# Kernel tuning notes

Measured on AMD Instinct MI355X. Metric: run time of the kernel, lower is better.

## Reference

```python
import jax, jax.numpy as jnp
import numpy as np

B, N, C = 2, 4096, 1024   # batch, input_size (seq), channels
H, Dh = 16, 64            # nhead, head_dim = channels // nhead
K = 256                   # dim_k (Linformer projected length)
FF = 4096                 # dim_ff
DEPTH = 2
EPS = 1e-5


def setup_inputs() -> dict:
    key = jax.random.key(0)
    ks = jax.random.split(key, 16)
    s = 0.02
    return {
        "x": jax.random.normal(ks[0], (B, N, C), jnp.float32),
        # per-layer, per-head Q/K/V projections: Linear(channels -> head_dim, bias=False)
        "Wq": jax.random.normal(ks[1], (DEPTH, H, C, Dh), jnp.float32) * s,
        "Wk": jax.random.normal(ks[2], (DEPTH, H, C, Dh), jnp.float32) * s,
        "Wv": jax.random.normal(ks[3], (DEPTH, H, C, Dh), jnp.float32) * s,
        # output proj: Linear(nhead*head_dim -> channels) with bias
        "Wo": jax.random.normal(ks[4], (DEPTH, H * Dh, C), jnp.float32) * s,
        "bo": jax.random.normal(ks[5], (DEPTH, C), jnp.float32) * s,
        # layerwise-shared E_proj = Linear(input_size -> dim_k) applied along seq axis
        # (same object used for both K and V projections)
        "Ew": jax.random.normal(ks[6], (K, N), jnp.float32) * (1.0 / np.sqrt(N)),
        "Eb": jax.random.normal(ks[7], (K,), jnp.float32) * s,
        # FeedForward: Linear(C->FF), gelu, Linear(FF->C)
        "W1": jax.random.normal(ks[8], (DEPTH, C, FF), jnp.float32) * s,
        "b1": jax.random.normal(ks[9], (DEPTH, FF), jnp.float32) * s,
        "W2": jax.random.normal(ks[10], (DEPTH, FF, C), jnp.float32) * s,
        "b2": jax.random.normal(ks[11], (DEPTH, C), jnp.float32) * s,
        # post-residual LayerNorm params: [layer, {attn, ff}, channels]
        "ln_g": 1.0 + 0.02 * jax.random.normal(ks[12], (DEPTH, 2, C), jnp.float32),
        "ln_b": 0.02 * jax.random.normal(ks[13], (DEPTH, 2, C), jnp.float32),
    }


def _layernorm(x, g, b):
    mu = jnp.mean(x, axis=-1, keepdims=True)
    var = jnp.var(x, axis=-1, keepdims=True)
    return (x - mu) * jax.lax.rsqrt(var + EPS) * g + b


def reference(x, Wq, Wk, Wv, Wo, bo, Ew, Eb, W1, b1, W2, b2, ln_g, ln_b):
    scale = 1.0 / np.sqrt(Dh)
    for l in range(DEPTH):
        # ---- Linformer multi-head attention (dropout = identity at inference) ----
        q = jnp.einsum('bnc,hcd->bhnd', x, Wq[l])   # [B,H,N,Dh]
        k = jnp.einsum('bnc,hcd->bhnd', x, Wk[l])
        v = jnp.einsum('bnc,hcd->bhnd', x, Wv[l])
        # project seq axis n -> k with shared E_proj (K^T @ E, V^T @ E)
        kp = jnp.einsum('bhnd,kn->bhkd', k, Ew) + Eb[None, None, :, None]  # [B,H,K,Dh]
        vp = jnp.einsum('bhnd,kn->bhkd', v, Ew) + Eb[None, None, :, None]
        p = jax.nn.softmax(jnp.einsum('bhnd,bhkd->bhnk', q, kp) * scale, axis=-1)
        o = jnp.einsum('bhnk,bhkd->bhnd', p, vp)
        o = o.transpose(0, 2, 1, 3).reshape(B, N, H * Dh)  # concat heads
        attn_out = o @ Wo[l] + bo[l]
        x = _layernorm(x + attn_out, ln_g[l, 0], ln_b[l, 0])  # Residual post-norm
        # ---- FeedForward ----
        h = jax.nn.gelu(x @ W1[l] + b1[l], approximate=False)
        ff_out = h @ W2[l] + b2[l]
        x = _layernorm(x + ff_out, ln_g[l, 1], ln_b[l, 1])
    return x
```

## Files before the change

### kernel.cpp

```cpp
#include <hip/hip_runtime.h>
#include <hip/hip_bf16.h>
#include <math.h>

typedef __bf16 bf16x8 __attribute__((ext_vector_type(8)));
typedef float f32x4 __attribute__((ext_vector_type(4)));

__global__ void cvt_f32_bf16(const float* __restrict__ in, __bf16* __restrict__ out, long n) {
    long i = ((long)blockIdx.x * 256 + threadIdx.x) * 4;
    long stride = (long)gridDim.x * 1024;
    for (; i < n; i += stride) {
        float4 v = *(const float4*)(in + i);
        out[i + 0] = (__bf16)v.x;
        out[i + 1] = (__bf16)v.y;
        out[i + 2] = (__bf16)v.z;
        out[i + 3] = (__bf16)v.w;
    }
}

__global__ void transpose_cvt(const float* __restrict__ in, __bf16* __restrict__ out,
                              int ldin, int ldout, long inBS, long outBS) {
    __shared__ __bf16 tile[32][33];
    in  += (long)blockIdx.z * inBS;
    out += (long)blockIdx.z * outBS;
    int n0 = blockIdx.x * 32, m0 = blockIdx.y * 32;
    for (int i = threadIdx.y; i < 32; i += 8)
        tile[i][threadIdx.x] = (__bf16)in[(long)(m0 + i) * ldin + n0 + threadIdx.x];
    __syncthreads();
    for (int i = threadIdx.y; i < 32; i += 8)
        out[(long)(n0 + i) * ldout + m0 + threadIdx.x] = tile[threadIdx.x][i];
}

__global__ void transpose_bf16(const __bf16* __restrict__ in, __bf16* __restrict__ out,
                               int rows, int cols) {
    __shared__ __bf16 tile[32][33];
    in  += (long)blockIdx.z * rows * cols;
    out += (long)blockIdx.z * rows * cols;
    int c0 = blockIdx.x * 32, r0 = blockIdx.y * 32;
    for (int i = threadIdx.y; i < 32; i += 8)
        tile[i][threadIdx.x] = in[(long)(r0 + i) * cols + c0 + threadIdx.x];
    __syncthreads();
    for (int i = threadIdx.y; i < 32; i += 8)
        out[(long)(c0 + i) * rows + r0 + threadIdx.x] = tile[threadIdx.x][i];
}

template<bool COLB, bool GELUF, bool RES, int OUT>
__global__ __launch_bounds__(512, 2) void gemm8p(
    const __bf16* __restrict__ A, int lda,
    const __bf16* __restrict__ Bt, int ldb,
    void* __restrict__ outp, int ldc,
    const float* __restrict__ colBias,
    const float* __restrict__ res, int ldres,
    int K)
{
    __shared__ __bf16 Asm[2][16384];
    __shared__ __bf16 Bsm[2][16384];

    const int tid = threadIdx.x, lane = tid & 63, wave = tid >> 6;
    const int l15 = lane & 15, l4 = lane >> 4;
    const int wm = wave >> 2, wn = wave & 3;

    int bx, by;
    {
        int id = blockIdx.y * gridDim.x + blockIdx.x;
        int xcd = id & 7, j = id >> 3;
        bx = (xcd & 3) * 8 + (j & 7);
        by = (xcd >> 2) * (gridDim.y >> 1) + (j >> 3);
    }
    const long m0 = (long)bx * 256, n0 = (long)by * 256;

    const int srow = wave * 16 + (lane >> 3);
    const int scol = ((lane & 7) ^ (lane >> 3)) << 3;
    const __bf16* Abp = A + (m0 + srow) * (long)lda + scol;
    const __bf16* Bbp = Bt + (n0 + srow) * (long)ldb + scol;

    const int NT = K >> 6;

    auto stageA = [&](int half, int tau) {
        const __bf16* s = Abp + (long)half * 128 * lda + (long)tau * 64;
        __bf16* d = &Asm[tau & 1][(half * 128 + wave * 16) * 64];
#pragma unroll
        for (int j = 0; j < 2; j++)
            __builtin_amdgcn_global_load_lds(
                (const __attribute__((address_space(1))) unsigned int*)(s + (long)j * 8 * lda),
                (__attribute__((address_space(3))) unsigned int*)(d + j * 512), 16, 0, 0);
    };
    auto stageB = [&](int half, int tau) {
        const __bf16* s = Bbp + (long)half * 128 * ldb + (long)tau * 64;
        __bf16* d = &Bsm[tau & 1][(half * 128 + wave * 16) * 64];
#pragma unroll
        for (int j = 0; j < 2; j++)
            __builtin_amdgcn_global_load_lds(
                (const __attribute__((address_space(1))) unsigned int*)(s + (long)j * 8 * ldb),
                (__attribute__((address_space(3))) unsigned int*)(d + j * 512), 16, 0, 0);
    };
    auto ldA = [&](int buf, int mi, int kk) -> bf16x8 {
        return *(const bf16x8*)&Asm[buf][(wm * 128 + mi * 16 + l15) * 64 + (((kk * 4 + l4) ^ (l15 & 7)) << 3)];
    };
    auto ldB = [&](int buf, int ni, int kk) -> bf16x8 {
        return *(const bf16x8*)&Bsm[buf][(wn * 64 + ni * 16 + l15) * 64 + (((kk * 4 + l4) ^ (l15 & 7)) << 3)];
    };

    f32x4 acc[8][4];
#pragma unroll
    for (int mi = 0; mi < 8; mi++)
#pragma unroll
        for (int ni = 0; ni < 4; ni++) acc[mi][ni] = (f32x4){0.f, 0.f, 0.f, 0.f};

    stageB(0, 0); stageB(1, 0); stageA(0, 0); stageA(1, 0);
    if (NT > 1) { stageB(0, 1); stageB(1, 1); }
    __builtin_amdgcn_sched_barrier(0);
    asm volatile("s_waitcnt vmcnt(4)" ::: "memory");
    __builtin_amdgcn_sched_barrier(0);
    __builtin_amdgcn_s_barrier();

    bf16x8 Breg[2][4];
    const int NI = K >> 7;
    for (int it = 0; it < NI; ++it) {
        const int T = it << 1;
        const bool last = (it == NI - 1);
#pragma unroll
        for (int p = 0; p < 8; ++p) {
            const int cb = p >> 2;
            const int q = p & 3;
            if (q == 0) {
#pragma unroll
                for (int kk = 0; kk < 2; kk++)
#pragma unroll
                    for (int ni = 0; ni < 4; ni++)
                        Breg[kk][ni] = ldB(cb, ni, kk);
            }
            bf16x8 a00 = ldA(cb, 2 * q, 0),     a01 = ldA(cb, 2 * q, 1);
            bf16x8 a10 = ldA(cb, 2 * q + 1, 0), a11 = ldA(cb, 2 * q + 1, 1);
            if      (p == 0) { stageA(0, T + 1); }
            else if (p == 1) { stageA(1, T + 1); }
            else if (p == 2) { if (T + 2 < NT) stageB(0, T + 2); }
            else if (p == 3) { if (T + 2 < NT) stageB(1, T + 2); }
            else if (p == 4) { if (T + 2 < NT) stageA(0, T + 2); }
            else if (p == 5) { if (T + 2 < NT) stageA(1, T + 2); }
            else if (p == 6) { if (T + 3 < NT) stageB(0, T + 3); }
            else             { if (T + 3 < NT) stageB(1, T + 3); }
            __builtin_amdgcn_sched_barrier(0);
            __builtin_amdgcn_s_barrier();
            __builtin_amdgcn_s_setprio(1);
#pragma unroll
            for (int ni = 0; ni < 4; ni++) {
                acc[2 * q][ni]     = __builtin_amdgcn_mfma_f32_16x16x32_bf16(a00, Breg[0][ni], acc[2 * q][ni], 0, 0, 0);
                acc[2 * q + 1][ni] = __builtin_amdgcn_mfma_f32_16x16x32_bf16(a10, Breg[0][ni], acc[2 * q + 1][ni], 0, 0, 0);
            }
#pragma unroll
            for (int ni = 0; ni < 4; ni++) {
                acc[2 * q][ni]     = __builtin_amdgcn_mfma_f32_16x16x32_bf16(a01, Breg[1][ni], acc[2 * q][ni], 0, 0, 0);
                acc[2 * q + 1][ni] = __builtin_amdgcn_mfma_f32_16x16x32_bf16(a11, Breg[1][ni], acc[2 * q + 1][ni], 0, 0, 0);
            }
            __builtin_amdgcn_s_setprio(0);
            if (p == 3) {
                if (last) { asm volatile("s_waitcnt vmcnt(0)" ::: "memory"); }
                else      { asm volatile("s_waitcnt vmcnt(4)" ::: "memory"); }
            } else if (p == 7 && !last) {
                asm volatile("s_waitcnt vmcnt(4)" ::: "memory");
            }
            __builtin_amdgcn_sched_barrier(0);
            __builtin_amdgcn_s_barrier();
        }
    }

    float* outf = (float*)outp;
    __bf16* outb = (__bf16*)outp;
#pragma unroll
    for (int mi = 0; mi < 8; mi++)
#pragma unroll
        for (int ni = 0; ni < 4; ni++) {
            long gmb = m0 + wm * 128 + mi * 16 + l4 * 4;
            long gc  = n0 + wn * 64 + ni * 16 + l15;
#pragma unroll
            for (int i = 0; i < 4; i++) {
                long gm = gmb + i;
                float v = acc[mi][ni][i];
                if (COLB)  v += colBias[gc];
                if (GELUF) v = 0.5f * v * (1.f + erff(v * 0.70710678118f));
                if (RES)   v += res[gm * (long)ldres + gc];
                if (OUT == 0) outf[gm * (long)ldc + gc] = v;
                else          outb[gm * (long)ldc + gc] = (__bf16)v;
            }
        }
}

template<bool ROWB, bool COLB, bool GELUF, bool RES, int OUT>
__global__ __launch_bounds__(256, 2) void gemm_bf16(
    const __bf16* __restrict__ A, int lda, long aBS,
    const __bf16* __restrict__ Bt, int ldb, long bBS,
    void* __restrict__ outp, int ldc, long cBS,
    const float* __restrict__ rowBias,
    const float* __restrict__ colBias,
    const float* __restrict__ res, int ldres,
    int K)
{
    __shared__ __bf16 Asm[128 * 64];
    __shared__ __bf16 Bsm[128 * 64];
    const int tid = threadIdx.x;
    const int lane = tid & 63, wave = tid >> 6;
    const int wm = wave >> 1, wn = wave & 1;
    const int l15 = lane & 15, l4 = lane >> 4;

    int bx = blockIdx.x, by = blockIdx.y;
    {
        int nwg = gridDim.x * gridDim.y;
        if ((nwg & 7) == 0) {
            int id = by * gridDim.x + bx;
            int cpx = nwg >> 3;
            int swz = (id & 7) * cpx + (id >> 3);
            bx = swz % gridDim.x;
            by = swz / gridDim.x;
        }
    }
    const long m0 = (long)bx * 128, n0 = (long)by * 128;
    A  += (long)blockIdx.z * aBS;
    Bt += (long)blockIdx.z * bBS;

    const int srow8 = lane >> 3;
    const int gunit = ((lane & 7) ^ srow8) << 3;
    const __bf16* Abase = A  + (m0 + wave * 8 + srow8) * (long)lda + gunit;
    const __bf16* Bbase = Bt + (n0 + wave * 8 + srow8) * (long)ldb + gunit;
    __bf16* AsmW = Asm + wave * 8 * 64;
    __bf16* BsmW = Bsm + wave * 8 * 64;
    const int swz_r = l15 & 7;

    f32x4 acc[4][4];
#pragma unroll
    for (int mi = 0; mi < 4; mi++)
#pragma unroll
        for (int ni = 0; ni < 4; ni++) acc[mi][ni] = (f32x4){0.f, 0.f, 0.f, 0.f};

    for (int k0 = 0; k0 < K; k0 += 64) {
        __syncthreads();
#pragma unroll
        for (int p = 0; p < 4; p++) {
            __builtin_amdgcn_global_load_lds(
                (const __attribute__((address_space(1))) unsigned int*)(Abase + (long)p * 32 * lda + k0),
                (__attribute__((address_space(3))) unsigned int*)(AsmW + p * 32 * 64), 16, 0, 0);
            __builtin_amdgcn_global_load_lds(
                (const __attribute__((address_space(1))) unsigned int*)(Bbase + (long)p * 32 * ldb + k0),
                (__attribute__((address_space(3))) unsigned int*)(BsmW + p * 32 * 64), 16, 0, 0);
        }
        asm volatile("s_waitcnt vmcnt(0)" ::: "memory");
        __syncthreads();
#pragma unroll
        for (int ks = 0; ks < 2; ks++) {
            bf16x8 af[4], bfv[4];
#pragma unroll
            for (int mi = 0; mi < 4; mi++)
                af[mi] = *(const bf16x8*)(Asm + (wm * 64 + mi * 16 + l15) * 64 + (((ks * 4 + l4) ^ swz_r) << 3));
#pragma unroll
            for (int ni = 0; ni < 4; ni++)
                bfv[ni] = *(const bf16x8*)(Bsm + (wn * 64 + ni * 16 + l15) * 64 + (((ks * 4 + l4) ^ swz_r) << 3));
#pragma unroll
            for (int mi = 0; mi < 4; mi++)
#pragma unroll
                for (int ni = 0; ni < 4; ni++)
                    acc[mi][ni] = __builtin_amdgcn_mfma_f32_16x16x32_bf16(af[mi], bfv[ni], acc[mi][ni], 0, 0, 0);
        }
    }

    float* outf = (float*)outp;
    __bf16* outb = (__bf16*)outp;
    const long cOff = (long)blockIdx.z * cBS;
#pragma unroll
    for (int mi = 0; mi < 4; mi++)
#pragma unroll
        for (int ni = 0; ni < 4; ni++) {
            long gmb = m0 + wm * 64 + mi * 16 + l4 * 4;
            long gc  = n0 + wn * 64 + ni * 16 + l15;
#pragma unroll
            for (int i = 0; i < 4; i++) {
                long gm = gmb + i;
                float v = acc[mi][ni][i];
                if (ROWB)  v += rowBias[gm];
                if (COLB)  v += colBias[gc];
                if (GELUF) v = 0.5f * v * (1.f + erff(v * 0.70710678118f));
                if (RES)   v += res[gm * (long)ldres + gc];
                if (OUT == 0)      outf[cOff + gm * (long)ldc + gc] = v;
                else if (OUT == 1) outb[cOff + gm * (long)ldc + gc] = (__bf16)v;
                else               outb[cOff + gc * (long)ldc + gm] = (__bf16)v;
            }
        }
}

__global__ __launch_bounds__(256, 2) void gemm128_split(
    const __bf16* __restrict__ A, int lda, long aBS,
    const __bf16* __restrict__ Bt, int ldb, long bBS,
    float* __restrict__ P, long cBS, int ldc,
    int Ksplit, int S)
{
    __shared__ __bf16 Asm[128 * 64];
    __shared__ __bf16 Bsm[128 * 64];
    const int tid = threadIdx.x;
    const int lane = tid & 63, wave = tid >> 6;
    const int wm = wave >> 1, wn = wave & 1;
    const int l15 = lane & 15, l4 = lane >> 4;
    const long m0 = (long)blockIdx.x * 128, n0 = (long)blockIdx.y * 128;
    const long zb = blockIdx.z / S;
    const int  sp = blockIdx.z % S;
    A  += zb * aBS + (long)sp * Ksplit;
    Bt += zb * bBS + (long)sp * Ksplit;

    const int srow8 = lane >> 3;
    const int gunit = ((lane & 7) ^ srow8) << 3;
    const __bf16* Abase = A + (m0 + wave * 8 + srow8) * (long)lda + gunit;
    const __bf16* Bbase = Bt + (n0 + wave * 8 + srow8) * (long)ldb + gunit;
    __bf16* AsmW = Asm + wave * 8 * 64;
    __bf16* BsmW = Bsm + wave * 8 * 64;
    const int swz_r = l15 & 7;

    f32x4 acc[4][4];
#pragma unroll
    for (int mi = 0; mi < 4; mi++)
#pragma unroll
        for (int ni = 0; ni < 4; ni++) acc[mi][ni] = (f32x4){0.f, 0.f, 0.f, 0.f};

    for (int k0 = 0; k0 < Ksplit; k0 += 64) {
        __syncthreads();
#pragma unroll
        for (int p = 0; p < 4; p++) {
            __builtin_amdgcn_global_load_lds(
                (const __attribute__((address_space(1))) unsigned int*)(Abase + (long)p * 32 * lda + k0),
                (__attribute__((address_space(3))) unsigned int*)(AsmW + p * 32 * 64), 16, 0, 0);
            __builtin_amdgcn_global_load_lds(
                (const __attribute__((address_space(1))) unsigned int*)(Bbase + (long)p * 32 * ldb + k0),
                (__attribute__((address_space(3))) unsigned int*)(BsmW + p * 32 * 64), 16, 0, 0);
        }
        asm volatile("s_waitcnt vmcnt(0)" ::: "memory");
        __syncthreads();
#pragma unroll
        for (int ks = 0; ks < 2; ks++) {
            bf16x8 af[4], bfv[4];
#pragma unroll
            for (int mi = 0; mi < 4; mi++)
                af[mi] = *(const bf16x8*)(Asm + (wm * 64 + mi * 16 + l15) * 64 + (((ks * 4 + l4) ^ swz_r) << 3));
#pragma unroll
            for (int ni = 0; ni < 4; ni++)
                bfv[ni] = *(const bf16x8*)(Bsm + (wn * 64 + ni * 16 + l15) * 64 + (((ks * 4 + l4) ^ swz_r) << 3));
#pragma unroll
            for (int mi = 0; mi < 4; mi++)
#pragma unroll
                for (int ni = 0; ni < 4; ni++)
                    acc[mi][ni] = __builtin_amdgcn_mfma_f32_16x16x32_bf16(af[mi], bfv[ni], acc[mi][ni], 0, 0, 0);
        }
    }

    float* out = P + (long)blockIdx.z * cBS;
#pragma unroll
    for (int mi = 0; mi < 4; mi++)
#pragma unroll
        for (int ni = 0; ni < 4; ni++) {
            long gmb = m0 + wm * 64 + mi * 16 + l4 * 4;
            long gc  = n0 + wn * 64 + ni * 16 + l15;
#pragma unroll
            for (int i = 0; i < 4; i++)
                out[(gmb + i) * (long)ldc + gc] = acc[mi][ni][i];
        }
}

template<bool BIAS, bool TRANS>
__global__ __launch_bounds__(256) void reduce_partials(
    const float* __restrict__ P, __bf16* __restrict__ out,
    const float* __restrict__ bias, int S, int M, int N, long pBS)
{
    int b = blockIdx.z;
    long idx = ((long)blockIdx.x * 256 + threadIdx.x) * 4;
    if (idx >= (long)M * N) return;
    const float* Pb = P + (long)b * S * pBS + idx;
    float4 a = *(const float4*)Pb;
    for (int s = 1; s < S; s++) {
        float4 v = *(const float4*)(Pb + (long)s * pBS);
        a.x += v.x; a.y += v.y; a.z += v.z; a.w += v.w;
    }
    int m = (int)(idx / N), n = (int)(idx % N);
    if (BIAS) { float bv = bias[m]; a.x += bv; a.y += bv; a.z += bv; a.w += bv; }
    float av[4] = {a.x, a.y, a.z, a.w};
    if (!TRANS) {
        __bf16* o = out + (long)b * M * N + idx;
        o[0] = (__bf16)av[0]; o[1] = (__bf16)av[1]; o[2] = (__bf16)av[2]; o[3] = (__bf16)av[3];
    } else {
#pragma unroll
        for (int j = 0; j < 4; j++)
            out[(long)b * M * N + (long)(n + j) * M + m] = (__bf16)av[j];
    }
}

__global__ __launch_bounds__(256, 2) void attn_fused(
    const __bf16* __restrict__ Q, const __bf16* __restrict__ KP,
    const __bf16* __restrict__ VPt, __bf16* __restrict__ O)
{
    __shared__ __bf16 plds[4][4096];
    const int tid = threadIdx.x, lane = tid & 63, wave = tid >> 6;
    const int l15 = lane & 15, l4 = lane >> 4;
    const int h = blockIdx.y, b = blockIdx.z;
    const long row0 = (long)b * 4096 + (long)blockIdx.x * 64 + wave * 16;

    bf16x8 aq[2];
#pragma unroll
    for (int ks = 0; ks < 2; ks++)
        aq[ks] = *(const bf16x8*)(Q + (row0 + l15) * 1024 + h * 64 + ks * 32 + l4 * 8);

    f32x4 s[16];
#pragma unroll
    for (int f = 0; f < 16; f++) {
        f32x4 a = (f32x4){0.f, 0.f, 0.f, 0.f};
#pragma unroll
        for (int ks = 0; ks < 2; ks++) {
            bf16x8 bk = *(const bf16x8*)(KP + ((long)b * 256 + f * 16 + l15) * 1024 + h * 64 + ks * 32 + l4 * 8);
            a = __builtin_amdgcn_mfma_f32_16x16x32_bf16(aq[ks], bk, a, 0, 0, 0);
        }
        s[f] = a;
    }

    const float scale = 0.125f;
#pragma unroll
    for (int i = 0; i < 4; i++) {
        float m_ = -3.4e38f;
#pragma unroll
        for (int f = 0; f < 16; f++) { float v = s[f][i] * scale; s[f][i] = v; m_ = fmaxf(m_, v); }
#pragma unroll
        for (int msk = 1; msk < 16; msk <<= 1) m_ = fmaxf(m_, __shfl_xor(m_, msk));
        float su = 0.f;
#pragma unroll
        for (int f = 0; f < 16; f++) { float e = expf(s[f][i] - m_); s[f][i] = e; su += e; }
#pragma unroll
        for (int msk = 1; msk < 16; msk <<= 1) su += __shfl_xor(su, msk);
        float inv = 1.f / su;
#pragma unroll
        for (int f = 0; f < 16; f++) s[f][i] *= inv;
    }

    __bf16* pl = plds[wave];
#pragma unroll
    for (int f = 0; f < 16; f++)
#pragma unroll
        for (int i = 0; i < 4; i++) {
            int r = l4 * 4 + i, c = f * 16 + l15;
            int off = r * 256 + ((((c >> 3) ^ (r & 7)) << 3) | (c & 7));
            pl[off] = (__bf16)s[f][i];
        }

    f32x4 o[4];
#pragma unroll
    for (int f2 = 0; f2 < 4; f2++) o[f2] = (f32x4){0.f, 0.f, 0.f, 0.f};
#pragma unroll
    for (int ks = 0; ks < 8; ks++) {
        int kk = ks * 32 + l4 * 8;
        int off = l15 * 256 + (((kk >> 3) ^ (l15 & 7)) << 3);
        bf16x8 ap = *(const bf16x8*)(pl + off);
#pragma unroll
        for (int f2 = 0; f2 < 4; f2++) {
            bf16x8 bv = *(const bf16x8*)(VPt + ((long)b * 1024 + h * 64 + f2 * 16 + l15) * 256 + kk);
            o[f2] = __builtin_amdgcn_mfma_f32_16x16x32_bf16(ap, bv, o[f2], 0, 0, 0);
        }
    }
#pragma unroll
    for (int f2 = 0; f2 < 4; f2++)
#pragma unroll
        for (int i = 0; i < 4; i++)
            O[(row0 + l4 * 4 + i) * 1024 + h * 64 + f2 * 16 + l15] = (__bf16)o[f2][i];
}

__global__ __launch_bounds__(256) void ln_kernel(const float* __restrict__ y,
    const float* __restrict__ g, const float* __restrict__ b,
    float* __restrict__ xout, __bf16* __restrict__ xb)
{
    const int row = blockIdx.x;
    const int t = threadIdx.x;
    const float4 v = ((const float4*)(y + (long)row * 1024))[t];
    float s  = v.x + v.y + v.z + v.w;
    float ss = v.x * v.x + v.y * v.y + v.z * v.z + v.w * v.w;
#pragma unroll
    for (int m = 1; m < 64; m <<= 1) { s += __shfl_xor(s, m); ss += __shfl_xor(ss, m); }
    __shared__ float red[2][4];
    const int wave = t >> 6, lane = t & 63;
    if (lane == 0) { red[0][wave] = s; red[1][wave] = ss; }
    __syncthreads();
    s  = red[0][0] + red[0][1] + red[0][2] + red[0][3];
    ss = red[1][0] + red[1][1] + red[1][2] + red[1][3];
    const float mu = s * (1.f / 1024.f);
    const float var = ss * (1.f / 1024.f) - mu * mu;
    const float rs = rsqrtf(var + 1e-5f);
    const float4 gv = ((const float4*)g)[t];
    const float4 bv = ((const float4*)b)[t];
    float o0 = (v.x - mu) * rs * gv.x + bv.x;
    float o1 = (v.y - mu) * rs * gv.y + bv.y;
    float o2 = (v.z - mu) * rs * gv.z + bv.z;
    float o3 = (v.w - mu) * rs * gv.w + bv.w;
    float4 ov; ov.x = o0; ov.y = o1; ov.z = o2; ov.w = o3;
    ((float4*)(xout + (long)row * 1024))[t] = ov;
    __bf16* xr = xb + (long)row * 1024 + t * 4;
    xr[0] = (__bf16)o0; xr[1] = (__bf16)o1; xr[2] = (__bf16)o2; xr[3] = (__bf16)o3;
}

extern "C" void kernel_launch(void* const* d_in, const int* in_sizes, int n_in,
                              void* d_out, int out_size, void* d_ws, size_t ws_size,
                              hipStream_t stream) {
    const float* x   = (const float*)d_in[0];
    const float* Wq  = (const float*)d_in[1];
    const float* Wk  = (const float*)d_in[2];
    const float* Wv  = (const float*)d_in[3];
    const float* Wo  = (const float*)d_in[4];
    const float* bo  = (const float*)d_in[5];
    const float* Ew  = (const float*)d_in[6];
    const float* Eb  = (const float*)d_in[7];
    const float* W1  = (const float*)d_in[8];
    const float* b1  = (const float*)d_in[9];
    const float* W2  = (const float*)d_in[10];
    const float* b2  = (const float*)d_in[11];
    const float* lng = (const float*)d_in[12];
    const float* lnb = (const float*)d_in[13];
    float* xout = (float*)d_out;

    char* base = (char*)d_ws;
    size_t off = 0;
    auto alloc = [&](size_t bytes) { void* p = base + off; off += (bytes + 255) & ~(size_t)255; return p; };
    __bf16* Wqt = (__bf16*)alloc(2ll * 1024 * 1024 * 2);
    __bf16* Wkt = (__bf16*)alloc(2ll * 1024 * 1024 * 2);
    __bf16* Wvt = (__bf16*)alloc(2ll * 1024 * 1024 * 2);
    __bf16* Wot = (__bf16*)alloc(2ll * 1024 * 1024 * 2);
    __bf16* W1t = (__bf16*)alloc(2ll * 1024 * 4096 * 2);
    __bf16* W2t = (__bf16*)alloc(2ll * 1024 * 4096 * 2);
    __bf16* Ewb = (__bf16*)alloc(256ll * 4096 * 2);
    __bf16* xb  = (__bf16*)alloc(8192ll * 1024 * 2);
    __bf16* xbT = (__bf16*)alloc(2ll * 1024 * 4096 * 2);
    float*  y   = (float*) alloc(8192ll * 1024 * 4);
    __bf16* xp  = (__bf16*)alloc(2ll * 256 * 1024 * 2);
    __bf16* KPb = (__bf16*)alloc(2ll * 256 * 1024 * 2);
    __bf16* VPt = (__bf16*)alloc(2ll * 1024 * 256 * 2);
    __bf16* big = (__bf16*)alloc(8192ll * 4096 * 2);
    float*  xpP = (float*)big;
    float*  kpP = (float*)((char*)big + (16ll << 20));
    float*  vpP = (float*)((char*)big + (24ll << 20));
    __bf16* Qb  = big;
    __bf16* Ob  = big + (16ll << 20);
    __bf16* hbuf = big;

    cvt_f32_bf16<<<2048, 256, 0, stream>>>(x, xb, 8388608);
    cvt_f32_bf16<<<1024, 256, 0, stream>>>(Ew, Ewb, 1048576);
    transpose_cvt<<<dim3(2, 32, 32),  dim3(32, 8), 0, stream>>>(Wq, Wqt, 64, 1024, 65536, 65536);
    transpose_cvt<<<dim3(2, 32, 32),  dim3(32, 8), 0, stream>>>(Wk, Wkt, 64, 1024, 65536, 65536);
    transpose_cvt<<<dim3(2, 32, 32),  dim3(32, 8), 0, stream>>>(Wv, Wvt, 64, 1024, 65536, 65536);
    transpose_cvt<<<dim3(32, 32, 2),  dim3(32, 8), 0, stream>>>(Wo, Wot, 1024, 1024, 1048576, 1048576);
    transpose_cvt<<<dim3(128, 32, 2), dim3(32, 8), 0, stream>>>(W1, W1t, 4096, 1024, 4194304, 4194304);
    transpose_cvt<<<dim3(32, 128, 2), dim3(32, 8), 0, stream>>>(W2, W2t, 1024, 4096, 4194304, 4194304);

    for (int l = 0; l < 2; l++) {
        const __bf16* Wqt_l = Wqt + (long)l * 1048576;
        const __bf16* Wkt_l = Wkt + (long)l * 1048576;
        const __bf16* Wvt_l = Wvt + (long)l * 1048576;
        const __bf16* Wot_l = Wot + (long)l * 1048576;
        const __bf16* W1t_l = W1t + (long)l * 4194304;
        const __bf16* W2t_l = W2t + (long)l * 4194304;
        const float* res = (l == 0) ? x : xout;

        transpose_bf16<<<dim3(32, 128, 2), dim3(32, 8), 0, stream>>>(xb, xbT, 4096, 1024);
        gemm128_split<<<dim3(2, 8, 16), 256, 0, stream>>>(
            Ewb, 4096, 0, xbT, 4096, 4194304, xpP, 262144, 1024, 512, 8);
        reduce_partials<false, false><<<dim3(256, 1, 2), 256, 0, stream>>>(
            xpP, xp, nullptr, 8, 256, 1024, 262144);
        gemm128_split<<<dim3(2, 8, 8), 256, 0, stream>>>(
            xp, 1024, 262144, Wkt_l, 1024, 0, kpP, 262144, 1024, 256, 4);
        reduce_partials<true, false><<<dim3(256, 1, 2), 256, 0, stream>>>(
            kpP, KPb, Eb, 4, 256, 1024, 262144);
        gemm128_split<<<dim3(2, 8, 8), 256, 0, stream>>>(
            xp, 1024, 262144, Wvt_l, 1024, 0, vpP, 262144, 1024, 256, 4);
        reduce_partials<true, true><<<dim3(256, 1, 2), 256, 0, stream>>>(
            vpP, VPt, Eb, 4, 256, 1024, 262144);
        gemm_bf16<false, false, false, false, 1><<<dim3(64, 8, 1), 256, 0, stream>>>(
            xb, 1024, 0, Wqt_l, 1024, 0, (void*)Qb, 1024, 0, nullptr, nullptr, nullptr, 0, 1024);
        attn_fused<<<dim3(64, 16, 2), 256, 0, stream>>>(Qb, KPb, VPt, Ob);
        gemm_bf16<false, true, false, true, 0><<<dim3(64, 8, 1), 256, 0, stream>>>(
            Ob, 1024, 0, Wot_l, 1024, 0, (void*)y, 1024, 0,
            nullptr, bo + l * 1024, res, 1024, 1024);
        ln_kernel<<<8192, 256, 0, stream>>>(y, lng + (2 * l + 0) * 1024, lnb + (2 * l + 0) * 1024, xout, xb);
        gemm8p<true, true, false, 1><<<dim3(32, 16), 512, 0, stream>>>(
            xb, 1024, W1t_l, 1024, (void*)hbuf, 4096, b1 + l * 4096, nullptr, 0, 1024);
        gemm8p<true, false, true, 0><<<dim3(32, 4), 512, 0, stream>>>(
            hbuf, 4096, W2t_l, 4096, (void*)y, 1024, b2 + l * 1024, xout, 1024, 4096);
        ln_kernel<<<8192, 256, 0, stream>>>(y, lng + (2 * l + 1) * 1024, lnb + (2 * l + 1) * 1024, xout, xb);
    }
}
```

Baseline: 907.4 us.

## Rework block-to-XCD tile swizzles and route FF2 GEMM through 128-tile kernel

Replaces the hardcoded XCD swizzle in the 256x256 GEMM with a generic mapping that places 4x4 tile patches on each XCD for L2 reuse. It also adds an explicit lgkmcnt wait after the barrier. The 128x128 GEMM gets a similar 8x8 patch-per-XCD mapping when grid sizes allow. The FF2 GEMM (K=4096, 128 blocks of 256x256) switches to the 128x128 kernel with 512 blocks, aiming for better CU occupancy at the cost of lower per-block reuse.

```diff
diff --git a/kernel.cpp b/kernel.cpp
--- a/kernel.cpp
+++ b/kernel.cpp
@@ -59,44 +59,50 @@
     const int l15 = lane & 15, l4 = lane >> 4;
     const int wm = wave >> 2, wn = wave & 3;
 
-    int bx, by;
+    int bx = blockIdx.x, by = blockIdx.y;
     {
-        int id = blockIdx.y * gridDim.x + blockIdx.x;
-        int xcd = id & 7, j = id >> 3;
-        bx = (xcd & 3) * 8 + (j & 7);
-        by = (xcd >> 2) * (gridDim.y >> 1) + (j >> 3);
+        int gx = gridDim.x, gy = gridDim.y, nb = gx * gy;
+        if ((gx & 3) == 0 && (gy & 3) == 0 && (nb & 127) == 0) {
+            int id = by * gx + bx;
+            int xcd = id & 7, local = id >> 3;
+            int ppc = nb >> 7;
+            int t = local >> 4, within = local & 15;
+            int pid = xcd * ppc + t;
+            int ppx = gx >> 2;
+            int pgy = pid / ppx, pgx = pid % ppx;
+            bx = pgx * 4 + (within & 3);
+            by = pgy * 4 + (within >> 2);
+        }
     }
     const long m0 = (long)bx * 256, n0 = (long)by * 256;
 
-    const int srow = wave * 16 + (lane >> 3);
-    const int scol = ((lane & 7) ^ (lane >> 3)) << 3;
-    const __bf16* Abp = A + (m0 + srow) * (long)lda + scol;
-    const __bf16* Bbp = Bt + (n0 + srow) * (long)ldb + scol;
-
-    const int NT = K >> 6;
-
-    auto stageA = [&](int half, int tau) {
+    const int srw = lane >> 3;
+    const int scol = ((lane & 7) ^ srw) << 3;
+    const __bf16* Abp = A  + (m0 + wave * 16 + srw) * (long)lda + scol;
+    const __bf16* Bbp = Bt + (n0 + wave * 16 + srw) * (long)ldb + scol;
+
+    auto stA = [&](int buf, int half, int tau) {
         const __bf16* s = Abp + (long)half * 128 * lda + (long)tau * 64;
-        __bf16* d = &Asm[tau & 1][(half * 128 + wave * 16) * 64];
+        __bf16* d = &Asm[buf][(half * 128 + wave * 16) * 64];
 #pragma unroll
         for (int j = 0; j < 2; j++)
             __builtin_amdgcn_global_load_lds(
                 (const __attribute__((address_space(1))) unsigned int*)(s + (long)j * 8 * lda),
                 (__attribute__((address_space(3))) unsigned int*)(d + j * 512), 16, 0, 0);
     };
-    auto stageB = [&](int half, int tau) {
+    auto stB = [&](int buf, int half, int tau) {
         const __bf16* s = Bbp + (long)half * 128 * ldb + (long)tau * 64;
-        __bf16* d = &Bsm[tau & 1][(half * 128 + wave * 16) * 64];
+        __bf16* d = &Bsm[buf][(half * 128 + wave * 16) * 64];
 #pragma unroll
         for (int j = 0; j < 2; j++)
             __builtin_amdgcn_global_load_lds(
                 (const __attribute__((address_space(1))) unsigned int*)(s + (long)j * 8 * ldb),
                 (__attribute__((address_space(3))) unsigned int*)(d + j * 512), 16, 0, 0);
     };
-    auto ldA = [&](int buf, int mi, int kk) -> bf16x8 {
+    auto ldAf = [&](int buf, int mi, int kk) -> bf16x8 {
         return *(const bf16x8*)&Asm[buf][(wm * 128 + mi * 16 + l15) * 64 + (((kk * 4 + l4) ^ (l15 & 7)) << 3)];
     };
-    auto ldB = [&](int buf, int ni, int kk) -> bf16x8 {
+    auto ldBf = [&](int buf, int ni, int kk) -> bf16x8 {
         return *(const bf16x8*)&Bsm[buf][(wn * 64 + ni * 16 + l15) * 64 + (((kk * 4 + l4) ^ (l15 & 7)) << 3)];
     };
 
@@ -106,41 +112,43 @@
 #pragma unroll
         for (int ni = 0; ni < 4; ni++) acc[mi][ni] = (f32x4){0.f, 0.f, 0.f, 0.f};
 
-    stageB(0, 0); stageB(1, 0); stageA(0, 0); stageA(1, 0);
-    if (NT > 1) { stageB(0, 1); stageB(1, 1); }
+    const int NT = K >> 6, NI = K >> 7;
+    stB(0, 0, 0); stB(0, 1, 0); stA(0, 0, 0); stA(0, 1, 0);
+    stB(1, 0, 1); stB(1, 1, 1);
     __builtin_amdgcn_sched_barrier(0);
     asm volatile("s_waitcnt vmcnt(4)" ::: "memory");
     __builtin_amdgcn_sched_barrier(0);
     __builtin_amdgcn_s_barrier();
 
     bf16x8 Breg[2][4];
-    const int NI = K >> 7;
     for (int it = 0; it < NI; ++it) {
         const int T = it << 1;
         const bool last = (it == NI - 1);
 #pragma unroll
         for (int p = 0; p < 8; ++p) {
-            const int cb = p >> 2;
+            const int buf = p >> 2;
             const int q = p & 3;
             if (q == 0) {
 #pragma unroll
                 for (int kk = 0; kk < 2; kk++)
 #pragma unroll
                     for (int ni = 0; ni < 4; ni++)
-                        Breg[kk][ni] = ldB(cb, ni, kk);
+                        Breg[kk][ni] = ldBf(buf, ni, kk);
             }
-            bf16x8 a00 = ldA(cb, 2 * q, 0),     a01 = ldA(cb, 2 * q, 1);
-            bf16x8 a10 = ldA(cb, 2 * q + 1, 0), a11 = ldA(cb, 2 * q + 1, 1);
-            if      (p == 0) { stageA(0, T + 1); }
-            else if (p == 1) { stageA(1, T + 1); }
-            else if (p == 2) { if (T + 2 < NT) stageB(0, T + 2); }
-            else if (p == 3) { if (T + 2 < NT) stageB(1, T + 2); }
-            else if (p == 4) { if (T + 2 < NT) stageA(0, T + 2); }
-            else if (p == 5) { if (T + 2 < NT) stageA(1, T + 2); }
-            else if (p == 6) { if (T + 3 < NT) stageB(0, T + 3); }
-            else             { if (T + 3 < NT) stageB(1, T + 3); }
+            bf16x8 a00 = ldAf(buf, 2 * q, 0),     a01 = ldAf(buf, 2 * q, 1);
+            bf16x8 a10 = ldAf(buf, 2 * q + 1, 0), a11 = ldAf(buf, 2 * q + 1, 1);
+            if      (p == 0) { stA(1, 0, T + 1); }
+            else if (p == 1) { stA(1, 1, T + 1); }
+            else if (p == 2) { if (!last) stB(0, 0, T + 2); }
+            else if (p == 3) { if (!last) stB(0, 1, T + 2); }
+            else if (p == 4) { if (!last) stA(0, 0, T + 2); }
+            else if (p == 5) { if (!last) stA(0, 1, T + 2); }
+            else if (p == 6) { if (!last) stB(1, 0, T + 3); }
+            else             { if (!last) stB(1, 1, T + 3); }
             __builtin_amdgcn_sched_barrier(0);
             __builtin_amdgcn_s_barrier();
+            asm volatile("s_waitcnt lgkmcnt(0)" ::: "memory");
+            __builtin_amdgcn_sched_barrier(0);
             __builtin_amdgcn_s_setprio(1);
 #pragma unroll
             for (int ni = 0; ni < 4; ni++) {
@@ -204,13 +212,24 @@
 
     int bx = blockIdx.x, by = blockIdx.y;
     {
-        int nwg = gridDim.x * gridDim.y;
-        if ((nwg & 7) == 0) {
-            int id = by * gridDim.x + bx;
-            int cpx = nwg >> 3;
+        int gx = gridDim.x, gy = gridDim.y;
+        int nb = gx * gy;
+        if ((gx & 7) == 0 && (gy & 7) == 0 && (nb & 511) == 0) {
+            int id = by * gx + bx;
+            int xcd = id & 7, local = id >> 3;
+            int t = local >> 6, within = local & 63;
+            int ppx = gx >> 3;
+            int ppc = nb >> 9;
+            int pid = xcd * ppc + t;
+            int pgy = pid / ppx, pgx = pid % ppx;
+            bx = pgx * 8 + (within & 7);
+            by = pgy * 8 + (within >> 3);
+        } else if ((nb & 7) == 0) {
+            int id = by * gx + bx;
+            int cpx = nb >> 3;
             int swz = (id & 7) * cpx + (id >> 3);
-            bx = swz % gridDim.x;
-            by = swz / gridDim.x;
+            bx = swz % gx;
+            by = swz / gx;
         }
     }
     const long m0 = (long)bx * 128, n0 = (long)by * 128;
@@ -578,8 +597,9 @@
         ln_kernel<<<8192, 256, 0, stream>>>(y, lng + (2 * l + 0) * 1024, lnb + (2 * l + 0) * 1024, xout, xb);
         gemm8p<true, true, false, 1><<<dim3(32, 16), 512, 0, stream>>>(
             xb, 1024, W1t_l, 1024, (void*)hbuf, 4096, b1 + l * 4096, nullptr, 0, 1024);
-        gemm8p<true, false, true, 0><<<dim3(32, 4), 512, 0, stream>>>(
-            hbuf, 4096, W2t_l, 4096, (void*)y, 1024, b2 + l * 1024, xout, 1024, 4096);
+        gemm_bf16<false, true, false, true, 0><<<dim3(64, 8, 1), 256, 0, stream>>>(
+            hbuf, 4096, 0, W2t_l, 4096, 0, (void*)y, 1024, 0,
+            nullptr, b2 + l * 1024, xout, 1024, 4096);
         ln_kernel<<<8192, 256, 0, stream>>>(y, lng + (2 * l + 1) * 1024, lnb + (2 * l + 1) * 1024, xout, xb);
     }
 }
```

Measured after the change: 809.8 us. 1.12x faster.
